# Kernel optimization log

Hardware: AMD Instinct MI355X
Metric: run time of the kernel (lower is better)

## Reference

```python
import jax, jax.numpy as jnp
import numpy as np

B, T, D = 2, 2048, 1024
H, DH = 16, 64


def setup_inputs() -> dict:
    key = jax.random.key(0)
    ks = jax.random.split(key, 8)
    return {
        "x": jax.random.normal(ks[0], (B, T, D), dtype=jnp.float32),
        "mask": jnp.ones((1, 1, T, T), dtype=bool),
        "Wq": jax.random.normal(ks[1], (D, D), dtype=jnp.float32) * 0.02,
        "Wk": jax.random.normal(ks[2], (D, D), dtype=jnp.float32) * 0.02,
        "Wv": jax.random.normal(ks[3], (D, D), dtype=jnp.float32) * 0.02,
        "Wo": jax.random.normal(ks[4], (D, D), dtype=jnp.float32) * 0.02,
        "S_q": jax.random.normal(ks[5], (H, DH, DH), dtype=jnp.float32),
        "S_k": jax.random.normal(ks[6], (H, DH, DH), dtype=jnp.float32),
    }


def reference(x, mask, Wq, Wk, Wv, Wo, S_q, S_k):
    b, t, _ = x.shape
    scale = DH ** (-0.5)
    # nn.Linear applies x @ W.T; our Wq etc. are the Linear weight matrices.
    def split_heads(y):
        return y.reshape(b, t, H, DH).transpose(0, 2, 1, 3)  # (B,H,T,DH)

    Q = split_heads(x @ Wq.T)
    K = split_heads(x @ Wk.T)
    V = split_heads(x @ Wv.T)
    Qp = jnp.einsum('bhtd,hde->bhte', Q, S_q)
    Kp = jnp.einsum('bhtd,hde->bhte', K, S_k)
    scores = jnp.einsum('bhte,bhse->bhts', Qp, Kp) * scale  # (B,H,T,T)
    scores = jnp.where(mask, scores, -jnp.inf)
    attn = jax.nn.softmax(scores, axis=-1)
    out = jnp.einsum('bhts,bhsd->bhtd', attn, V)
    out = out.transpose(0, 2, 1, 3).reshape(b, t, D)
    return out @ Wo.T
```

## Files before the change

kernel.cpp:

```cpp
#include <hip/hip_runtime.h>
#include <cstdint>
#include <cmath>


#define B_   2
#define T_   2048
#define Dm   1024
#define H_   16
#define DH_  64
#define Ntok (B_ * T_)
#define ND   (Ntok * Dm)
#define DD   (Dm * Dm)
#define QKS  2048
#define PST  80

typedef _Float16 f16;
typedef _Float16 f16x4 __attribute__((ext_vector_type(4)));
typedef _Float16 f16x8 __attribute__((ext_vector_type(8)));
typedef float    f32x4 __attribute__((ext_vector_type(4)));

__device__ inline f32x4 mfma16(f16x8 a, f16x8 b, f32x4 c) {
  return __builtin_amdgcn_mfma_f32_16x16x32_f16(a, b, c, 0, 0, 0);
}

__device__ inline void async16(const void* g, void* l) {
  __builtin_amdgcn_global_load_lds(
      (const __attribute__((address_space(1))) unsigned int*)g,
      (__attribute__((address_space(3))) unsigned int*)l, 16, 0, 0);
}

__device__ inline float vmax4(f32x4 v) {
  return fmaxf(fmaxf(v[0], v[1]), fmaxf(v[2], v[3]));
}
__device__ inline float vsum4(f32x4 v) {
  return (v[0] + v[1]) + (v[2] + v[3]);
}

__global__ void cvt_all(const float* __restrict__ x, const float* __restrict__ Wv,
                        const float* __restrict__ Wo, f16* __restrict__ x_f,
                        f16* __restrict__ WvDst, f16* __restrict__ Wo_f) {
  int i = (blockIdx.x * 256 + threadIdx.x) * 4;
  const float* src;
  f16* dst;
  int off;
  if (i < ND) {
    src = x; dst = x_f; off = i;
  } else if (i < ND + DD) {
    src = Wv; dst = WvDst; off = i - ND;
  } else {
    src = Wo; dst = Wo_f; off = i - ND - DD;
  }
  f32x4 v = *(const f32x4*)(src + off);
  f16x4 o;
#pragma unroll
  for (int j = 0; j < 4; ++j) o[j] = (f16)v[j];
  *(f16x4*)(dst + off) = o;
}

__global__ __launch_bounds__(64) void fold_w2(
    const float* __restrict__ Wq, const float* __restrict__ Sq,
    const float* __restrict__ Wk, const float* __restrict__ Sk,
    f16* __restrict__ T) {
  __shared__ __align__(16) float sS[64 * 64];
  const int tid = threadIdx.x;
  const int hy = blockIdx.y;
  const float* W = (hy < 16) ? Wq : Wk;
  const float* S = (hy < 16) ? Sq : Sk;
  f16* out = T + (size_t)((hy < 16) ? 0 : 1024) * Dm;
  const int h = hy & 15;
  const int d = blockIdx.x * 64 + tid;
#pragma unroll 8
  for (int i = 0; i < 64; ++i) sS[i * 64 + tid] = S[h * 4096 + i * 64 + tid];
  __syncthreads();
  float acc[64];
#pragma unroll
  for (int e = 0; e < 64; ++e) acc[e] = 0.f;
  for (int c = 0; c < 64; ++c) {
    float wv = W[(size_t)(h * 64 + c) * Dm + d];
    const f32x4* srow = (const f32x4*)&sS[c * 64];
#pragma unroll
    for (int e4 = 0; e4 < 16; ++e4) {
      f32x4 sv = srow[e4];
      acc[e4 * 4 + 0] += wv * sv[0];
      acc[e4 * 4 + 1] += wv * sv[1];
      acc[e4 * 4 + 2] += wv * sv[2];
      acc[e4 * 4 + 3] += wv * sv[3];
    }
  }
#pragma unroll
  for (int e = 0; e < 64; ++e)
    out[(size_t)(h * 64 + e) * Dm + d] = (f16)acc[e];
}

template <int OUTMODE, int TN>
__global__ __launch_bounds__(256) void gemm_bt(
    const f16* __restrict__ A, const f16* __restrict__ B,
    float* __restrict__ Cf, f16* __restrict__ Ch, f16* __restrict__ Ct,
    int M, int N, int K) {
  constexpr int AS = 128 * 32;
  constexpr int BS = TN * 32;
  constexpr int MT = (TN == 128) ? 4 : 2;
  extern __shared__ __align__(16) f16 smem[];

  const int tid = threadIdx.x;
  const int w = tid >> 6, lane = tid & 63, g = lane >> 4, ln = lane & 15;
  const int wm = (TN == 128) ? (w >> 1) * 64 : w * 32;
  const int wn = (TN == 128) ? (w & 1) * 64 : 0;
  const int bm = blockIdx.y * 128, bn = blockIdx.x * TN;

  f32x4 acc[MT][4] = {};
  const int r0 = tid >> 2;
  const int kb = (tid & 3) * 8;

  auto issue = [&](int kc, int buf) {
    f16* dA = smem + buf * AS;
    f16* dB = smem + 2 * AS + buf * BS;
#pragma unroll
    for (int i = 0; i < 2; ++i) {
      size_t aoff = (size_t)(bm + i * 64 + r0) * K + kc + kb;
      int lo = i * 4096 + w * 1024;
      async16(A + aoff, (char*)dA + lo);
      if (TN == 128 || i == 0) {
        size_t boff = (size_t)(bn + i * 64 + r0) * K + kc + kb;
        async16(B + boff, (char*)dB + lo);
      }
    }
  };

  issue(0, 0);
  const int KI = K / 32;
  for (int i = 0; i < KI; ++i) {
    __syncthreads();
    if (i + 1 < KI) issue((i + 1) * 32, (i + 1) & 1);
    const f16* cA = smem + (i & 1) * AS;
    const f16* cB = smem + 2 * AS + (i & 1) * BS;
    f16x8 af[MT];
#pragma unroll
    for (int mt = 0; mt < MT; ++mt)
      af[mt] = *(const f16x8*)&cA[(wm + mt * 16 + ln) * 32 + g * 8];
#pragma unroll
    for (int nt = 0; nt < 4; ++nt) {
      f16x8 bf = *(const f16x8*)&cB[(wn + nt * 16 + ln) * 32 + g * 8];
#pragma unroll
      for (int mt = 0; mt < MT; ++mt)
        acc[mt][nt] = mfma16(af[mt], bf, acc[mt][nt]);
    }
  }

  if (OUTMODE == 3 && bn >= 2048) {
#pragma unroll
    for (int mt = 0; mt < MT; ++mt)
#pragma unroll
      for (int nt = 0; nt < 4; ++nt) {
        int ch = bn - 2048 + wn + nt * 16 + ln;
        size_t base = (size_t)ch * Ntok + bm + wm + mt * 16 + g * 4;
        f16x4 ov;
#pragma unroll
        for (int r = 0; r < 4; ++r) ov[r] = (f16)acc[mt][nt][r];
        *(f16x4*)&Ct[base] = ov;
      }
    return;
  }
#pragma unroll
  for (int mt = 0; mt < MT; ++mt)
#pragma unroll
    for (int nt = 0; nt < 4; ++nt)
#pragma unroll
      for (int r = 0; r < 4; ++r) {
        int row = bm + wm + mt * 16 + g * 4 + r;
        int col = bn + wn + nt * 16 + ln;
        float v = acc[mt][nt][r];
        if (OUTMODE == 0) {
          Cf[(size_t)row * N + col] = v;
        } else {
          Ch[(size_t)row * QKS + col] = (f16)v;
        }
      }
}

__global__ __launch_bounds__(512) void flash_attn(
    const f16* __restrict__ QK, const f16* __restrict__ Vt,
    f16* __restrict__ Op, float* __restrict__ Mp, float* __restrict__ Lp) {
  __shared__ __align__(16) f16 sKV[2 * 8192];
  __shared__ __align__(16) f16 sP[8 * 16 * PST];
  constexpr int VOFF = 4096;

  const int tid = threadIdx.x;
  const int w = tid >> 6, lane = tid & 63, g = lane >> 4, ln = lane & 15;
  const int bh = blockIdx.x, b = bh >> 4, h = bh & 15;
  const int sp = blockIdx.y;
  const int kbase = sp * (T_ / 2);
  const int q0 = blockIdx.z * 256 + w * 32;
  const size_t rowBase = (size_t)b * T_;
  const int hc = h * DH_;

  f16x8 qf[2][2];
#pragma unroll
  for (int t = 0; t < 2; ++t) {
    size_t qrow = (rowBase + q0 + t * 16 + ln) * (size_t)QKS + hc;
#pragma unroll
    for (int s = 0; s < 2; ++s) {
      f16x8 q = *(const f16x8*)(QK + qrow + s * 32 + g * 8);
#pragma unroll
      for (int j = 0; j < 8; ++j) q[j] *= (f16)0.1803368801111244f;
      qf[t][s] = q;
    }
  }

  float mrow[2] = {-INFINITY, -INFINITY}, lrow[2] = {0.f, 0.f};
  f32x4 oacc[2][4] = {};

  const int srow = tid >> 3;
  const int sel = ((tid & 7) * 8) ^ ((srow & 7) * 8);

  auto issue = [&](int kc, int buf) {
    char* base = (char*)sKV + buf * 16384;
    size_t koff = (rowBase + kc + srow) * (size_t)QKS + 1024 + hc + sel;
    async16(QK + koff, base + tid * 16);
    size_t voff = (size_t)(hc + srow) * Ntok + rowBase + kc + sel;
    async16(Vt + voff, base + 8192 + tid * 16);
  };

  issue(kbase, 0);
  constexpr int NC = T_ / 2 / 64;
  for (int i = 0; i < NC; ++i) {
    __syncthreads();
    if (i + 1 < NC) issue(kbase + (i + 1) * 64, (i + 1) & 1);
    const f16* cK = sKV + (i & 1) * 8192;
    const f16* cVT = cK + VOFF;

    const int c0 = (g * 8) ^ ((ln & 7) * 8);
    const int c1 = (32 + g * 8) ^ ((ln & 7) * 8);

    f32x4 s4[2][4];
#pragma unroll
    for (int nt = 0; nt < 4; ++nt) {
      int row = (nt * 16 + ln) * 64;
      f16x8 k80 = *(const f16x8*)&cK[row + c0];
      f16x8 k81 = *(const f16x8*)&cK[row + c1];
#pragma unroll
      for (int t = 0; t < 2; ++t) {
        f32x4 a = {};
        a = mfma16(k80, qf[t][0], a);
        a = mfma16(k81, qf[t][1], a);
        s4[t][nt] = a;
      }
    }

    f16* pw = sP + w * (16 * PST);
    f16x8 pb[2][2];
#pragma unroll
    for (int t = 0; t < 2; ++t) {
      f32x4 m4 = s4[t][0];
#pragma unroll
      for (int nt = 1; nt < 4; ++nt) {
        m4[0] = fmaxf(m4[0], s4[t][nt][0]);
        m4[1] = fmaxf(m4[1], s4[t][nt][1]);
        m4[2] = fmaxf(m4[2], s4[t][nt][2]);
        m4[3] = fmaxf(m4[3], s4[t][nt][3]);
      }
      float mx = vmax4(m4);
      mx = fmaxf(mx, __shfl_xor(mx, 16, 64));
      mx = fmaxf(mx, __shfl_xor(mx, 32, 64));
      float mn = fmaxf(mrow[t], mx);
      float alpha = __builtin_amdgcn_exp2f(mrow[t] - mn);
      mrow[t] = mn;
      f32x4 p4[4];
      f16x4 pk[4];
#pragma unroll
      for (int nt = 0; nt < 4; ++nt)
#pragma unroll
        for (int r = 0; r < 4; ++r) {
          float pv = __builtin_amdgcn_exp2f(s4[t][nt][r] - mn);
          p4[nt][r] = pv;
          pk[nt][r] = (f16)pv;
        }
      f32x4 sv4 = (p4[0] + p4[1]) + (p4[2] + p4[3]);
      float sum = vsum4(sv4);
      sum += __shfl_xor(sum, 16, 64);
      sum += __shfl_xor(sum, 32, 64);
      lrow[t] = lrow[t] * alpha + sum;
      if (__any(alpha != 1.0f)) {
#pragma unroll
        for (int dt = 0; dt < 4; ++dt) oacc[t][dt] *= alpha;
      }
#pragma unroll
      for (int nt = 0; nt < 4; ++nt)
        *(f16x4*)&pw[ln * PST + nt * 16 + g * 4] = pk[nt];
      asm volatile("" ::: "memory");
#pragma unroll
      for (int s = 0; s < 2; ++s)
        pb[t][s] = *(const f16x8*)&pw[ln * PST + s * 32 + g * 8];
      asm volatile("" ::: "memory");
    }

#pragma unroll
    for (int s = 0; s < 2; ++s) {
      int col = (s == 0) ? c0 : c1;
#pragma unroll
      for (int dt = 0; dt < 4; ++dt) {
        f16x8 va = *(const f16x8*)&cVT[(dt * 16 + ln) * 64 + col];
        oacc[0][dt] = mfma16(va, pb[0][s], oacc[0][dt]);
        oacc[1][dt] = mfma16(va, pb[1][s], oacc[1][dt]);
      }
    }
  }

#pragma unroll
  for (int t = 0; t < 2; ++t) {
    size_t q = rowBase + q0 + t * 16 + ln;
    size_t orow = ((size_t)sp * Ntok + q) * Dm + hc;
#pragma unroll
    for (int dt = 0; dt < 4; ++dt) {
      f16x4 ov;
#pragma unroll
      for (int r = 0; r < 4; ++r) ov[r] = (f16)oacc[t][dt][r];
      *(f16x4*)&Op[orow + dt * 16 + g * 4] = ov;
    }
    if (g == 0) {
      Mp[((size_t)sp * Ntok + q) * H_ + h] = mrow[t];
      Lp[((size_t)sp * Ntok + q) * H_ + h] = lrow[t];
    }
  }
}

__global__ void flash_combine(const f16* __restrict__ Op,
                              const float* __restrict__ Mp,
                              const float* __restrict__ Lp,
                              f16* __restrict__ AO) {
  int idx = blockIdx.x * 256 + threadIdx.x;
  int tok = idx >> 8;
  int c4 = idx & 255;
  int ch = c4 * 4;
  int h = ch >> 6;
  float m0 = Mp[(size_t)tok * H_ + h];
  float m1 = Mp[((size_t)Ntok + tok) * H_ + h];
  float l0 = Lp[(size_t)tok * H_ + h];
  float l1 = Lp[((size_t)Ntok + tok) * H_ + h];
  float mM = fmaxf(m0, m1);
  float a0 = __builtin_amdgcn_exp2f(m0 - mM);
  float a1 = __builtin_amdgcn_exp2f(m1 - mM);
  float rl = 1.0f / (a0 * l0 + a1 * l1);
  a0 *= rl;
  a1 *= rl;
  f16x4 o0 = *(const f16x4*)&Op[(size_t)tok * Dm + ch];
  f16x4 o1 = *(const f16x4*)&Op[((size_t)Ntok + tok) * Dm + ch];
  f16x4 ov;
#pragma unroll
  for (int r = 0; r < 4; ++r) ov[r] = (f16)(a0 * (float)o0[r] + a1 * (float)o1[r]);
  *(f16x4*)&AO[(size_t)tok * Dm + ch] = ov;
}

extern "C" void kernel_launch(void* const* d_in, const int* in_sizes, int n_in,
                              void* d_out, int out_size, void* d_ws, size_t ws_size,
                              hipStream_t stream) {
  const float* x  = (const float*)d_in[0];
  const float* Wq = (const float*)d_in[2];
  const float* Wk = (const float*)d_in[3];
  const float* Wv = (const float*)d_in[4];
  const float* Wo = (const float*)d_in[5];
  const float* Sq = (const float*)d_in[6];
  const float* Sk = (const float*)d_in[7];

  char* p = (char*)d_ws;
  auto alloc = [&](size_t bytes) {
    char* r = p;
    p += (bytes + 255) & ~(size_t)255;
    return r;
  };
  f16*   x_f  = (f16*)alloc((size_t)ND * 2);
  f16*   Wqkv = (f16*)alloc((size_t)3 * DD * 2);
  f16*   Wo_f = (f16*)alloc((size_t)DD * 2);
  f16*   QK   = (f16*)alloc((size_t)Ntok * QKS * 2);
  f16*   Vt_f = (f16*)alloc((size_t)ND * 2);
  f16*   AO   = (f16*)alloc((size_t)ND * 2);
  f16*   Op   = (f16*)alloc((size_t)2 * ND * 2);
  float* Mp   = (float*)alloc((size_t)2 * Ntok * H_ * 4);
  float* Lp   = (float*)alloc((size_t)2 * Ntok * H_ * 4);

  cvt_all<<<(ND + 2 * DD) / 1024, 256, 0, stream>>>(
      x, Wv, Wo, x_f, Wqkv + (size_t)2048 * Dm, Wo_f);
  fold_w2<<<dim3(16, 32), 64, 0, stream>>>(Wq, Sq, Wk, Sk, Wqkv);

  gemm_bt<3, 128><<<dim3(3072 / 128, Ntok / 128), 256, 32768, stream>>>(
      x_f, Wqkv, nullptr, QK, Vt_f, Ntok, 3072, Dm);

  flash_attn<<<dim3(B_ * H_, 2, T_ / 256), 512, 0, stream>>>(QK, Vt_f,
                                                             Op, Mp, Lp);
  flash_combine<<<ND / 1024, 256, 0, stream>>>(Op, Mp, Lp, AO);

  gemm_bt<0, 64><<<dim3(Dm / 64, Ntok / 128), 256, 24576, stream>>>(
      AO, Wo_f, (float*)d_out, nullptr, nullptr, Ntok, Dm, Dm);
}
```

Baseline: 232.1 us.

## Split attention keys four ways and swizzle P scratch instead of padding

```diff
diff --git a/kernel.cpp b/kernel.cpp
--- a/kernel.cpp
+++ b/kernel.cpp
@@ -12,7 +12,8 @@
 #define ND   (Ntok * Dm)
 #define DD   (Dm * Dm)
 #define QKS  2048
-#define PST  80
+#define NSP  4
+#define KSP  (T_ / NSP)
 
 typedef _Float16 f16;
 typedef _Float16 f16x4 __attribute__((ext_vector_type(4)));
@@ -182,14 +183,14 @@
     const f16* __restrict__ QK, const f16* __restrict__ Vt,
     f16* __restrict__ Op, float* __restrict__ Mp, float* __restrict__ Lp) {
   __shared__ __align__(16) f16 sKV[2 * 8192];
-  __shared__ __align__(16) f16 sP[8 * 16 * PST];
+  __shared__ __align__(16) f16 sP[8 * 16 * 64];
   constexpr int VOFF = 4096;
 
   const int tid = threadIdx.x;
   const int w = tid >> 6, lane = tid & 63, g = lane >> 4, ln = lane & 15;
   const int bh = blockIdx.x, b = bh >> 4, h = bh & 15;
   const int sp = blockIdx.y;
-  const int kbase = sp * (T_ / 2);
+  const int kbase = sp * KSP;
   const int q0 = blockIdx.z * 256 + w * 32;
   const size_t rowBase = (size_t)b * T_;
   const int hc = h * DH_;
@@ -222,15 +223,16 @@
   };
 
   issue(kbase, 0);
-  constexpr int NC = T_ / 2 / 64;
+  constexpr int NC = KSP / 64;
   for (int i = 0; i < NC; ++i) {
     __syncthreads();
     if (i + 1 < NC) issue(kbase + (i + 1) * 64, (i + 1) & 1);
     const f16* cK = sKV + (i & 1) * 8192;
     const f16* cVT = cK + VOFF;
 
-    const int c0 = (g * 8) ^ ((ln & 7) * 8);
-    const int c1 = (32 + g * 8) ^ ((ln & 7) * 8);
+    const int swz = (ln & 7) * 8;
+    const int c0 = (g * 8) ^ swz;
+    const int c1 = (32 + g * 8) ^ swz;
 
     f32x4 s4[2][4];
 #pragma unroll
@@ -247,7 +249,7 @@
       }
     }
 
-    f16* pw = sP + w * (16 * PST);
+    f16* pw = sP + w * (16 * 64);
     f16x8 pb[2][2];
 #pragma unroll
     for (int t = 0; t < 2; ++t) {
@@ -286,11 +288,11 @@
       }
 #pragma unroll
       for (int nt = 0; nt < 4; ++nt)
-        *(f16x4*)&pw[ln * PST + nt * 16 + g * 4] = pk[nt];
+        *(f16x4*)&pw[ln * 64 + ((nt * 16 + g * 4) ^ swz)] = pk[nt];
       asm volatile("" ::: "memory");
 #pragma unroll
       for (int s = 0; s < 2; ++s)
-        pb[t][s] = *(const f16x8*)&pw[ln * PST + s * 32 + g * 8];
+        pb[t][s] = *(const f16x8*)&pw[ln * 64 + ((s * 32 + g * 8) ^ swz)];
       asm volatile("" ::: "memory");
     }
 
@@ -333,21 +335,32 @@
   int c4 = idx & 255;
   int ch = c4 * 4;
   int h = ch >> 6;
-  float m0 = Mp[(size_t)tok * H_ + h];
-  float m1 = Mp[((size_t)Ntok + tok) * H_ + h];
-  float l0 = Lp[(size_t)tok * H_ + h];
-  float l1 = Lp[((size_t)Ntok + tok) * H_ + h];
-  float mM = fmaxf(m0, m1);
-  float a0 = __builtin_amdgcn_exp2f(m0 - mM);
-  float a1 = __builtin_amdgcn_exp2f(m1 - mM);
-  float rl = 1.0f / (a0 * l0 + a1 * l1);
-  a0 *= rl;
-  a1 *= rl;
-  f16x4 o0 = *(const f16x4*)&Op[(size_t)tok * Dm + ch];
-  f16x4 o1 = *(const f16x4*)&Op[((size_t)Ntok + tok) * Dm + ch];
+  float m[NSP], l[NSP];
+  float mM = -INFINITY;
+#pragma unroll
+  for (int s = 0; s < NSP; ++s) {
+    m[s] = Mp[((size_t)s * Ntok + tok) * H_ + h];
+    l[s] = Lp[((size_t)s * Ntok + tok) * H_ + h];
+    mM = fmaxf(mM, m[s]);
+  }
+  float a[NSP], den = 0.f;
+#pragma unroll
+  for (int s = 0; s < NSP; ++s) {
+    a[s] = __builtin_amdgcn_exp2f(m[s] - mM);
+    den += a[s] * l[s];
+  }
+  float rl = 1.0f / den;
+  float acc[4] = {0.f, 0.f, 0.f, 0.f};
+#pragma unroll
+  for (int s = 0; s < NSP; ++s) {
+    f16x4 o = *(const f16x4*)&Op[((size_t)s * Ntok + tok) * Dm + ch];
+    float ws = a[s] * rl;
+#pragma unroll
+    for (int r = 0; r < 4; ++r) acc[r] += ws * (float)o[r];
+  }
   f16x4 ov;
 #pragma unroll
-  for (int r = 0; r < 4; ++r) ov[r] = (f16)(a0 * (float)o0[r] + a1 * (float)o1[r]);
+  for (int r = 0; r < 4; ++r) ov[r] = (f16)acc[r];
   *(f16x4*)&AO[(size_t)tok * Dm + ch] = ov;
 }
 
@@ -374,9 +387,9 @@
   f16*   QK   = (f16*)alloc((size_t)Ntok * QKS * 2);
   f16*   Vt_f = (f16*)alloc((size_t)ND * 2);
   f16*   AO   = (f16*)alloc((size_t)ND * 2);
-  f16*   Op   = (f16*)alloc((size_t)2 * ND * 2);
-  float* Mp   = (float*)alloc((size_t)2 * Ntok * H_ * 4);
-  float* Lp   = (float*)alloc((size_t)2 * Ntok * H_ * 4);
+  f16*   Op   = (f16*)alloc((size_t)NSP * ND * 2);
+  float* Mp   = (float*)alloc((size_t)NSP * Ntok * H_ * 4);
+  float* Lp   = (float*)alloc((size_t)NSP * Ntok * H_ * 4);
 
   cvt_all<<<(ND + 2 * DD) / 1024, 256, 0, stream>>>(
       x, Wv, Wo, x_f, Wqkv + (size_t)2048 * Dm, Wo_f);
@@ -385,8 +398,8 @@
   gemm_bt<3, 128><<<dim3(3072 / 128, Ntok / 128), 256, 32768, stream>>>(
       x_f, Wqkv, nullptr, QK, Vt_f, Ntok, 3072, Dm);
 
-  flash_attn<<<dim3(B_ * H_, 2, T_ / 256), 512, 0, stream>>>(QK, Vt_f,
-                                                             Op, Mp, Lp);
+  flash_attn<<<dim3(B_ * H_, NSP, T_ / 256), 512, 0, stream>>>(QK, Vt_f,
+                                                               Op, Mp, Lp);
   flash_combine<<<ND / 1024, 256, 0, stream>>>(Op, Mp, Lp, AO);
 
   gemm_bt<0, 64><<<dim3(Dm / 64, Ntok / 128), 256, 24576, stream>>>(
```

New measurement: 231.5 us. No clear change (-0.3%).
